# Optimization experiments

Hardware: AMD Instinct MI355X
Metric: run time of the kernel (lower is better)

## Reference

```python
import jax, jax.numpy as jnp
import numpy as np
from jax import lax

T, E, H = 4096, 1024, 1024


def setup_inputs() -> dict:
    key = jax.random.key(0)
    ks = jax.random.split(key, 14)
    u = lambda k, shp: jax.random.uniform(k, shp, dtype=jnp.float32) * 0.02  # small so gates don't saturate
    return {
        "x": jax.random.normal(ks[0], (T, E), dtype=jnp.float32),
        "Uf": u(ks[1], (H, E)), "Wf": u(ks[2], (H, H)), "Bf": u(ks[3], (H,)),
        "Ug": u(ks[4], (H, E)), "Wg": u(ks[5], (H, H)), "Bg": u(ks[6], (H,)),
        "Uq": u(ks[7], (H, E)), "Wq": u(ks[8], (H, H)), "Bq": u(ks[9], (H,)),
        "U": u(ks[10], (H, E)), "W": u(ks[11], (H, H)), "B": u(ks[12], (H,)),
    }


def reference(x, Uf, Wf, Bf, Ug, Wg, Bg, Uq, Wq, Bq, U, W, B):
    hdim = Wf.shape[0]
    # Precompute all input projections in 4 big GEMMs: [T, H] each
    xf = x @ Uf.T + Bf
    xc = x @ U.T + B
    xg = x @ Ug.T + Bg
    xq = x @ Uq.T + Bq

    def step(carry, inp):
        h, s = carry
        xf_t, xc_t, xg_t, xq_t = inp
        f = jax.nn.sigmoid(Wf @ h + xf_t)
        c = jax.nn.sigmoid(W @ h + xc_t)   # note: original uses sigmoid (not tanh) for the candidate
        g = jax.nn.sigmoid(Wg @ h + xg_t)
        s = f * s + g * c
        q = jax.nn.sigmoid(Wq @ h + xq_t)
        h = jnp.tanh(s) * q
        return (h, s), h

    init = (jnp.zeros((hdim,), x.dtype), jnp.zeros((hdim,), x.dtype))
    _, out = lax.scan(step, init, (xf, xc, xg, xq))
    return out  # [T, H]
```

## Files before the change

### kernel.cpp

```cpp
#include <hip/hip_runtime.h>
#include <hip/hip_fp16.h>
#include <stdint.h>


#define T_STEPS 4096
#define HDIM 1024

typedef _Float16 half2v __attribute__((ext_vector_type(2)));

__device__ __forceinline__ float dot2(uint32_t a, uint32_t b, float c) {
#if __has_builtin(__builtin_amdgcn_fdot2)
  return __builtin_amdgcn_fdot2(__builtin_bit_cast(half2v, a),
                                __builtin_bit_cast(half2v, b), c, false);
#else
  half2v av = __builtin_bit_cast(half2v, a);
  half2v bv = __builtin_bit_cast(half2v, b);
  return c + (float)av.x * (float)bv.x + (float)av.y * (float)bv.y;
#endif
}

__global__ __launch_bounds__(256) void convw(const float* __restrict__ w0,
                                             const float* __restrict__ w1,
                                             const float* __restrict__ w2,
                                             const float* __restrict__ w3,
                                             __half* __restrict__ dst) {
  int i = (blockIdx.x * 256 + threadIdx.x) * 4;
  int g = i >> 20;
  int off = i & 1048575;
  const float* src = g == 0 ? w0 : g == 1 ? w1 : g == 2 ? w2 : w3;
  float4 v = *(const float4*)(src + off);
  union { __half h[4]; uint2 u; } cv;
  cv.h[0] = __float2half(v.x); cv.h[1] = __float2half(v.y);
  cv.h[2] = __float2half(v.z); cv.h[3] = __float2half(v.w);
  *(uint2*)(dst + i) = cv.u;
}

__global__ void zerok(uint32_t* __restrict__ p) {
  int i = blockIdx.x * 256 + threadIdx.x;
  if (i < 2048) p[i] = 0;
}

__global__ __launch_bounds__(256) void gemmk(
    const float* __restrict__ x,
    const float* __restrict__ u0, const float* __restrict__ u1,
    const float* __restrict__ u2, const float* __restrict__ u3,
    const float* __restrict__ b0, const float* __restrict__ b1,
    const float* __restrict__ b2, const float* __restrict__ b3,
    __half* __restrict__ xpre) {
  __shared__ float As[64][33];
  __shared__ float Bs[64][33];
  const int tid = threadIdx.x;
  const int m0 = blockIdx.y * 64;
  const int n0 = blockIdx.x * 64;
  const int g = n0 >> 10;
  const float* Up = g == 0 ? u0 : g == 1 ? u1 : g == 2 ? u2 : u3;
  const float* Bp = g == 0 ? b0 : g == 1 ? b1 : g == 2 ? b2 : b3;
  const int j0 = n0 & 1023;
  const int tx = tid & 15, ty = tid >> 4;
  const int lr = tid >> 3, lc = (tid & 7) << 2;
  float acc[4][4] = {};
  for (int k0 = 0; k0 < 1024; k0 += 32) {
    float4 a0 = *(const float4*)&x[(size_t)(m0 + lr) * 1024 + k0 + lc];
    float4 a1 = *(const float4*)&x[(size_t)(m0 + lr + 32) * 1024 + k0 + lc];
    float4 c0 = *(const float4*)&Up[(size_t)(j0 + lr) * 1024 + k0 + lc];
    float4 c1 = *(const float4*)&Up[(size_t)(j0 + lr + 32) * 1024 + k0 + lc];
    __syncthreads();
    As[lr][lc + 0] = a0.x; As[lr][lc + 1] = a0.y; As[lr][lc + 2] = a0.z; As[lr][lc + 3] = a0.w;
    As[lr + 32][lc + 0] = a1.x; As[lr + 32][lc + 1] = a1.y; As[lr + 32][lc + 2] = a1.z; As[lr + 32][lc + 3] = a1.w;
    Bs[lr][lc + 0] = c0.x; Bs[lr][lc + 1] = c0.y; Bs[lr][lc + 2] = c0.z; Bs[lr][lc + 3] = c0.w;
    Bs[lr + 32][lc + 0] = c1.x; Bs[lr + 32][lc + 1] = c1.y; Bs[lr + 32][lc + 2] = c1.z; Bs[lr + 32][lc + 3] = c1.w;
    __syncthreads();
#pragma unroll
    for (int k = 0; k < 32; ++k) {
      float a0v = As[ty * 4 + 0][k], a1v = As[ty * 4 + 1][k];
      float a2v = As[ty * 4 + 2][k], a3v = As[ty * 4 + 3][k];
      float b0v = Bs[tx * 4 + 0][k], b1v = Bs[tx * 4 + 1][k];
      float b2v = Bs[tx * 4 + 2][k], b3v = Bs[tx * 4 + 3][k];
      acc[0][0] += a0v * b0v; acc[0][1] += a0v * b1v; acc[0][2] += a0v * b2v; acc[0][3] += a0v * b3v;
      acc[1][0] += a1v * b0v; acc[1][1] += a1v * b1v; acc[1][2] += a1v * b2v; acc[1][3] += a1v * b3v;
      acc[2][0] += a2v * b0v; acc[2][1] += a2v * b1v; acc[2][2] += a2v * b2v; acc[2][3] += a2v * b3v;
      acc[3][0] += a3v * b0v; acc[3][1] += a3v * b1v; acc[3][2] += a3v * b2v; acc[3][3] += a3v * b3v;
    }
  }
#pragma unroll
  for (int i = 0; i < 4; ++i) {
    size_t rowi = (size_t)(m0 + ty * 4 + i);
#pragma unroll
    for (int j = 0; j < 4; ++j) {
      int jj = j0 + tx * 4 + j;
      float v = acc[i][j] + Bp[jj];
      xpre[rowi * 4096 + n0 + tx * 4 + j] = __float2half(v);
    }
  }
}

__global__ __launch_bounds__(512, 2) void rnnk(
    const __half* __restrict__ w16,
    const __half* __restrict__ xpre,
    uint32_t* tagged,
    float* __restrict__ out) {
  __shared__ uint32_t hl[4 * 132];
  __shared__ float gl[128];
  const int wg = blockIdx.x;
  const int tid = threadIdx.x;
  const int wave = tid >> 6, lane = tid & 63;
  const int g = wave >> 1;
  const int rloc = ((wave & 1) << 4) + (lane >> 2);
  const int row = (wg << 5) + rloc;
  const int c = lane & 3;
  const bool rowlead = (c == 0);
  const bool w0 = (wave == 0);

  uint32_t wv[128];
  {
    const uint4* wp = reinterpret_cast<const uint4*>(
        w16 + ((size_t)g << 20) + ((size_t)row << 10) + (c << 8));
#pragma unroll
    for (int i = 0; i < 32; ++i) {
      uint4 w4 = wp[i];
      wv[4 * i + 0] = w4.x; wv[4 * i + 1] = w4.y;
      wv[4 * i + 2] = w4.z; wv[4 * i + 3] = w4.w;
    }
  }
#pragma unroll
  for (int j = 0; j < 128; ++j) asm volatile("" : "+v"(wv[j]));

  float s = 0.f;

  for (int t = 0; t < T_STEPS; ++t) {
    float xv = 0.f;
    if (rowlead)
      xv = __half2float(xpre[(size_t)t * 4096 + ((size_t)g << 10) + row]);

    if (w0) {
      const unsigned long long* pp =
          reinterpret_cast<const unsigned long long*>(tagged + ((t & 1) << 10)) +
          (lane << 3);
      const uint32_t tg = (uint32_t)t;
      unsigned long long v[8];
      bool ok;
      do {
#pragma unroll
        for (int j = 0; j < 8; ++j)
          v[j] = __hip_atomic_load(pp + j, __ATOMIC_RELAXED, __HIP_MEMORY_SCOPE_AGENT);
        ok = true;
#pragma unroll
        for (int j = 0; j < 8; ++j)
          ok = ok && (((uint32_t)(v[j] >> 16) & 0xffffu) == tg) &&
               (((uint32_t)(v[j] >> 48) & 0xffffu) == tg);
      } while (!ok);
      uint32_t pk[8];
#pragma unroll
      for (int j = 0; j < 8; ++j)
        pk[j] = (uint32_t)(v[j] & 0xffffu) | (((uint32_t)(v[j] >> 32) & 0xffffu) << 16);
      uint32_t* dst = &hl[132 * (lane >> 4) + ((lane << 3) & 127)];
      uint4 w1; w1.x = pk[0]; w1.y = pk[1]; w1.z = pk[2]; w1.w = pk[3];
      uint4 w2; w2.x = pk[4]; w2.y = pk[5]; w2.z = pk[6]; w2.w = pk[7];
      *reinterpret_cast<uint4*>(dst) = w1;
      *reinterpret_cast<uint4*>(dst + 4) = w2;
    }
    __syncthreads();

    float p = 0.f;
    const uint4* hp = reinterpret_cast<const uint4*>(&hl[132 * c]);
#pragma unroll
    for (int i = 0; i < 32; ++i) {
      uint4 h4 = hp[i];
      p = dot2(wv[4 * i + 0], h4.x, p);
      p = dot2(wv[4 * i + 1], h4.y, p);
      p = dot2(wv[4 * i + 2], h4.z, p);
      p = dot2(wv[4 * i + 3], h4.w, p);
    }
    p += __shfl_xor(p, 1);
    p += __shfl_xor(p, 2);

    if (rowlead) {
      float z = p + xv;
      gl[(g << 5) + rloc] = 1.f / (1.f + __expf(-z));
    }
    __syncthreads();

    if (w0 && lane < 32) {
      const int r = lane;
      float f = gl[r], cc = gl[32 + r], gg = gl[64 + r], q = gl[96 + r];
      s = f * s + gg * cc;
      float e2 = __expf(2.f * s);
      float th = 1.f - 2.f / (e2 + 1.f);
      float h = th * q;
      out[(size_t)t * HDIM + (wg << 5) + r] = h;
      uint32_t hb = (uint32_t)__half_as_ushort(__float2half(h));
      uint32_t dw = ((uint32_t)(t + 1) << 16) | hb;
      __hip_atomic_store(&tagged[(((t + 1) & 1) << 10) + (wg << 5) + r], dw,
                         __ATOMIC_RELAXED, __HIP_MEMORY_SCOPE_AGENT);
    }
  }
}

extern "C" void kernel_launch(void* const* d_in, const int* in_sizes, int n_in,
                              void* d_out, int out_size, void* d_ws, size_t ws_size,
                              hipStream_t stream) {
  const float* x  = (const float*)d_in[0];
  const float* Uf = (const float*)d_in[1];
  const float* Wf = (const float*)d_in[2];
  const float* Bf = (const float*)d_in[3];
  const float* Ug = (const float*)d_in[4];
  const float* Wg = (const float*)d_in[5];
  const float* Bg = (const float*)d_in[6];
  const float* Uq = (const float*)d_in[7];
  const float* Wq = (const float*)d_in[8];
  const float* Bq = (const float*)d_in[9];
  const float* U  = (const float*)d_in[10];
  const float* W  = (const float*)d_in[11];
  const float* B  = (const float*)d_in[12];
  float* out = (float*)d_out;

  char* ws = (char*)d_ws;
  __half* xpre = (__half*)ws;
  __half* w16 = (__half*)(ws + (size_t)32 * 1024 * 1024);
  uint32_t* tagged = (uint32_t*)(ws + (size_t)40 * 1024 * 1024);

  convw<<<4096, 256, 0, stream>>>(Wf, W, Wg, Wq, w16);
  zerok<<<8, 256, 0, stream>>>(tagged);
  gemmk<<<dim3(64, 64), 256, 0, stream>>>(x, Uf, U, Ug, Uq, Bf, B, Bg, Bq, xpre);
  rnnk<<<32, 512, 0, stream>>>(w16, xpre, tagged, out);
}
```

Baseline: 8.900 ms.

## Split recurrence across 64 workgroups with all four gates per row in one thread group

The recurrent kernel now runs on 64 workgroups of 16 rows each instead of 32 workgroups of 32 rows. Each group of 32 threads computes all four gate dot products for one hidden row, so the weights are repacked into a per-thread interleaved layout. This removes the second block barrier and the shared gate buffer, and the leader thread does the cell update directly. It also double-buffers the shared h vector and cuts register use to 64 weight registers per thread, at the cost of more workgroups polling the global sync flags and a longer shuffle reduction.

```diff
diff --git a/kernel.cpp b/kernel.cpp
--- a/kernel.cpp
+++ b/kernel.cpp
@@ -5,8 +5,10 @@
 
 #define T_STEPS 4096
 #define HDIM 1024
+#define NWG 64
 
 typedef _Float16 half2v __attribute__((ext_vector_type(2)));
+typedef uint32_t u32x4 __attribute__((ext_vector_type(4)));
 
 __device__ __forceinline__ float dot2(uint32_t a, uint32_t b, float c) {
 #if __has_builtin(__builtin_amdgcn_fdot2)
@@ -19,20 +21,26 @@
 #endif
 }
 
+__device__ __forceinline__ float sigf(float z) { return 1.f / (1.f + __expf(-z)); }
+
 __global__ __launch_bounds__(256) void convw(const float* __restrict__ w0,
                                              const float* __restrict__ w1,
                                              const float* __restrict__ w2,
                                              const float* __restrict__ w3,
-                                             __half* __restrict__ dst) {
-  int i = (blockIdx.x * 256 + threadIdx.x) * 4;
-  int g = i >> 20;
-  int off = i & 1048575;
+                                             uint32_t* __restrict__ dst) {
+  int o = blockIdx.x * 256 + threadIdx.x;
+  int i = o & 63;
+  int lg = o >> 6;
+  int wg = lg >> 9, tidl = lg & 511;
+  int k = tidl & 31, rloc = tidl >> 5;
+  int row = (wg << 4) + rloc;
+  int g = i >> 4, ic = i & 15;
+  int col = (k << 5) + (ic << 1);
   const float* src = g == 0 ? w0 : g == 1 ? w1 : g == 2 ? w2 : w3;
-  float4 v = *(const float4*)(src + off);
-  union { __half h[4]; uint2 u; } cv;
-  cv.h[0] = __float2half(v.x); cv.h[1] = __float2half(v.y);
-  cv.h[2] = __float2half(v.z); cv.h[3] = __float2half(v.w);
-  *(uint2*)(dst + i) = cv.u;
+  float2 v = *(const float2*)(src + (size_t)row * 1024 + col);
+  uint32_t dw = (uint32_t)__half_as_ushort(__float2half(v.x)) |
+                ((uint32_t)__half_as_ushort(__float2half(v.y)) << 16);
+  dst[o] = dw;
 }
 
 __global__ void zerok(uint32_t* __restrict__ p) {
@@ -95,46 +103,47 @@
 }
 
 __global__ __launch_bounds__(512, 2) void rnnk(
-    const __half* __restrict__ w16,
+    const uint32_t* __restrict__ wpack,
     const __half* __restrict__ xpre,
     uint32_t* tagged,
     float* __restrict__ out) {
-  __shared__ uint32_t hl[4 * 132];
-  __shared__ float gl[128];
+  __shared__ uint32_t hl[2][640];
   const int wg = blockIdx.x;
   const int tid = threadIdx.x;
   const int wave = tid >> 6, lane = tid & 63;
-  const int g = wave >> 1;
-  const int rloc = ((wave & 1) << 4) + (lane >> 2);
-  const int row = (wg << 5) + rloc;
-  const int c = lane & 3;
-  const bool rowlead = (c == 0);
+  const int k = tid & 31;
+  const int rloc = tid >> 5;
+  const int row = (wg << 4) + rloc;
   const bool w0 = (wave == 0);
-
-  uint32_t wv[128];
+  const bool leader = (k == 0);
+
+  u32x4 wv[16];
   {
-    const uint4* wp = reinterpret_cast<const uint4*>(
-        w16 + ((size_t)g << 20) + ((size_t)row << 10) + (c << 8));
-#pragma unroll
-    for (int i = 0; i < 32; ++i) {
-      uint4 w4 = wp[i];
-      wv[4 * i + 0] = w4.x; wv[4 * i + 1] = w4.y;
-      wv[4 * i + 2] = w4.z; wv[4 * i + 3] = w4.w;
-    }
-  }
-#pragma unroll
-  for (int j = 0; j < 128; ++j) asm volatile("" : "+v"(wv[j]));
+    const u32x4* wp = reinterpret_cast<const u32x4*>(wpack) +
+                      (((size_t)wg << 9) + (size_t)tid) * 16;
+#pragma unroll
+    for (int i = 0; i < 16; ++i) wv[i] = wp[i];
+  }
 
   float s = 0.f;
 
   for (int t = 0; t < T_STEPS; ++t) {
-    float xv = 0.f;
-    if (rowlead)
-      xv = __half2float(xpre[(size_t)t * 4096 + ((size_t)g << 10) + row]);
-
+#pragma unroll
+    for (int i = 0; i < 16; ++i) asm volatile("" : "+v"(wv[i]));
+
+    float xf = 0.f, xc = 0.f, xg = 0.f, xq = 0.f;
+    if (leader) {
+      const __half* xp = xpre + ((size_t)t << 12) + row;
+      xf = __half2float(xp[0]);
+      xc = __half2float(xp[1024]);
+      xg = __half2float(xp[2048]);
+      xq = __half2float(xp[3072]);
+    }
+
+    const int buf = t & 1;
     if (w0) {
       const unsigned long long* pp =
-          reinterpret_cast<const unsigned long long*>(tagged + ((t & 1) << 10)) +
+          reinterpret_cast<const unsigned long long*>(tagged + (buf << 10)) +
           (lane << 3);
       const uint32_t tg = (uint32_t)t;
       unsigned long long v[8];
@@ -147,50 +156,64 @@
 #pragma unroll
         for (int j = 0; j < 8; ++j)
           ok = ok && (((uint32_t)(v[j] >> 16) & 0xffffu) == tg) &&
-               (((uint32_t)(v[j] >> 48) & 0xffffu) == tg);
+               ((uint32_t)(v[j] >> 48) == tg);
       } while (!ok);
       uint32_t pk[8];
 #pragma unroll
       for (int j = 0; j < 8; ++j)
         pk[j] = (uint32_t)(v[j] & 0xffffu) | (((uint32_t)(v[j] >> 32) & 0xffffu) << 16);
-      uint32_t* dst = &hl[132 * (lane >> 4) + ((lane << 3) & 127)];
-      uint4 w1; w1.x = pk[0]; w1.y = pk[1]; w1.z = pk[2]; w1.w = pk[3];
-      uint4 w2; w2.x = pk[4]; w2.y = pk[5]; w2.z = pk[6]; w2.w = pk[7];
-      *reinterpret_cast<uint4*>(dst) = w1;
-      *reinterpret_cast<uint4*>(dst + 4) = w2;
+      uint32_t* dst = &hl[buf][20 * (lane >> 1) + ((lane & 1) << 3)];
+      u32x4 wA, wB;
+      wA.x = pk[0]; wA.y = pk[1]; wA.z = pk[2]; wA.w = pk[3];
+      wB.x = pk[4]; wB.y = pk[5]; wB.z = pk[6]; wB.w = pk[7];
+      *reinterpret_cast<u32x4*>(dst) = wA;
+      *reinterpret_cast<u32x4*>(dst + 4) = wB;
     }
     __syncthreads();
 
-    float p = 0.f;
-    const uint4* hp = reinterpret_cast<const uint4*>(&hl[132 * c]);
-#pragma unroll
-    for (int i = 0; i < 32; ++i) {
-      uint4 h4 = hp[i];
-      p = dot2(wv[4 * i + 0], h4.x, p);
-      p = dot2(wv[4 * i + 1], h4.y, p);
-      p = dot2(wv[4 * i + 2], h4.z, p);
-      p = dot2(wv[4 * i + 3], h4.w, p);
-    }
-    p += __shfl_xor(p, 1);
-    p += __shfl_xor(p, 2);
-
-    if (rowlead) {
-      float z = p + xv;
-      gl[(g << 5) + rloc] = 1.f / (1.f + __expf(-z));
-    }
-    __syncthreads();
-
-    if (w0 && lane < 32) {
-      const int r = lane;
-      float f = gl[r], cc = gl[32 + r], gg = gl[64 + r], q = gl[96 + r];
+    float a0 = 0.f, a1 = 0.f, a2 = 0.f, a3 = 0.f;
+    const uint32_t* hb = &hl[buf][20 * k];
+#pragma unroll
+    for (int m = 0; m < 4; ++m) {
+      u32x4 h4 = *reinterpret_cast<const u32x4*>(hb + (m << 2));
+      a0 = dot2(wv[m].x, h4.x, a0);
+      a0 = dot2(wv[m].y, h4.y, a0);
+      a0 = dot2(wv[m].z, h4.z, a0);
+      a0 = dot2(wv[m].w, h4.w, a0);
+      a1 = dot2(wv[4 + m].x, h4.x, a1);
+      a1 = dot2(wv[4 + m].y, h4.y, a1);
+      a1 = dot2(wv[4 + m].z, h4.z, a1);
+      a1 = dot2(wv[4 + m].w, h4.w, a1);
+      a2 = dot2(wv[8 + m].x, h4.x, a2);
+      a2 = dot2(wv[8 + m].y, h4.y, a2);
+      a2 = dot2(wv[8 + m].z, h4.z, a2);
+      a2 = dot2(wv[8 + m].w, h4.w, a2);
+      a3 = dot2(wv[12 + m].x, h4.x, a3);
+      a3 = dot2(wv[12 + m].y, h4.y, a3);
+      a3 = dot2(wv[12 + m].z, h4.z, a3);
+      a3 = dot2(wv[12 + m].w, h4.w, a3);
+    }
+#pragma unroll
+    for (int mk = 1; mk <= 16; mk <<= 1) {
+      a0 += __shfl_xor(a0, mk);
+      a1 += __shfl_xor(a1, mk);
+      a2 += __shfl_xor(a2, mk);
+      a3 += __shfl_xor(a3, mk);
+    }
+
+    if (leader) {
+      float f = sigf(a0 + xf);
+      float cc = sigf(a1 + xc);
+      float gg = sigf(a2 + xg);
+      float q = sigf(a3 + xq);
       s = f * s + gg * cc;
       float e2 = __expf(2.f * s);
       float th = 1.f - 2.f / (e2 + 1.f);
       float h = th * q;
-      out[(size_t)t * HDIM + (wg << 5) + r] = h;
-      uint32_t hb = (uint32_t)__half_as_ushort(__float2half(h));
-      uint32_t dw = ((uint32_t)(t + 1) << 16) | hb;
-      __hip_atomic_store(&tagged[(((t + 1) & 1) << 10) + (wg << 5) + r], dw,
+      out[(size_t)t * HDIM + row] = h;
+      uint32_t dw = ((uint32_t)(t + 1) << 16) |
+                    (uint32_t)__half_as_ushort(__float2half(h));
+      __hip_atomic_store(&tagged[(((t + 1) & 1) << 10) + row], dw,
                          __ATOMIC_RELAXED, __HIP_MEMORY_SCOPE_AGENT);
     }
   }
@@ -216,11 +239,11 @@
 
   char* ws = (char*)d_ws;
   __half* xpre = (__half*)ws;
-  __half* w16 = (__half*)(ws + (size_t)32 * 1024 * 1024);
+  uint32_t* wpack = (uint32_t*)(ws + (size_t)32 * 1024 * 1024);
   uint32_t* tagged = (uint32_t*)(ws + (size_t)40 * 1024 * 1024);
 
-  convw<<<4096, 256, 0, stream>>>(Wf, W, Wg, Wq, w16);
+  convw<<<8192, 256, 0, stream>>>(Wf, W, Wg, Wq, wpack);
   zerok<<<8, 256, 0, stream>>>(tagged);
   gemmk<<<dim3(64, 64), 256, 0, stream>>>(x, Uf, U, Ug, Uq, Bf, B, Bg, Bq, xpre);
-  rnnk<<<32, 512, 0, stream>>>(w16, xpre, tagged, out);
-}
+  rnnk<<<NWG, 512, 0, stream>>>(wpack, xpre, tagged, out);
+}
```

New measurement: 15.49 ms. 1.74x slower.
